# Kernel optimization log

Measured on AMD Instinct MI355X. Metric: run time of the kernel, lower is better.

Reference implementation:

```python
import jax, jax.numpy as jnp
import numpy as np

COLOR_SIZE = 4
SIZE = 64
FILTERS = 512
LENGTH = SIZE * SIZE * 3  # 12288


def setup_inputs() -> dict:
    key = jax.random.key(0)
    k1, k2, k3 = jax.random.split(key, 3)
    example = jax.random.randint(k1, (8, SIZE, SIZE, 3), 0, COLOR_SIZE, dtype=jnp.int32)
    kernel = jax.random.normal(k2, (FILTERS, LENGTH), dtype=jnp.float32)
    bias = jnp.zeros((FILTERS,), dtype=jnp.float32)
    dense_w = jax.random.normal(k3, (FILTERS, COLOR_SIZE), dtype=jnp.float32) * 0.02
    dense_b = jnp.zeros((COLOR_SIZE,), dtype=jnp.float32)
    return {"example": example, "kernel": kernel, "bias": bias,
            "dense_w": dense_w, "dense_b": dense_b}


def reference(example, kernel, bias, dense_w, dense_b):
    B = example.shape[0]
    L = kernel.shape[1]  # 12288
    # normalize int pixels to [-1, 1)
    x = example.astype(jnp.float32) / COLOR_SIZE * 2.0 - 1.0
    x = x.reshape(B, L)                                   # [B, L]
    # FFT-based long (causal full) convolution, fft_length = 2L
    Xf = jnp.fft.rfft(x, n=2 * L, axis=-1)                # [B, L+1] complex64
    Kf = jnp.fft.rfft(kernel, n=2 * L, axis=-1)           # [F, L+1]
    y = jnp.fft.irfft(Xf[:, None, :] * Kf[None, :, :], n=2 * L, axis=-1)[..., :L]  # [B, F, L]
    y = jnp.transpose(y, (0, 2, 1)) + bias                # [B, L, F]
    y = jax.nn.relu(y)
    out = y @ dense_w + dense_b                           # [B, L, color_size]
    return out.reshape(B, SIZE, SIZE, 3, COLOR_SIZE).astype(jnp.float32)
```

## Files before the change

kernel.cpp:

```cpp
#include <hip/hip_runtime.h>

#define FF 512
#define LL 12288
#define NJC 1556
#define NR 128

typedef _Float16 half8 __attribute__((ext_vector_type(8)));
typedef float    f32x4 __attribute__((ext_vector_type(4)));

__global__ __launch_bounds__(256) void build_At(const float* __restrict__ kern,
                                                _Float16* __restrict__ At) {
    int tid  = blockIdx.x * 256 + threadIdx.x;
    int lane = tid & 63;
    int rest = tid >> 6;
    int dc   = rest % 384;
    int ft   = rest / 384;
    int f    = ft * 16 + (lane & 15);
    int d0   = dc * 32 + (lane >> 4) * 8;
    const float* src = kern + (size_t)f * LL + d0;
    half8 v;
#pragma unroll
    for (int i = 0; i < 8; ++i) v[i] = (_Float16)src[i];
    ((half8*)At)[tid] = v;
}

__global__ __launch_bounds__(256) void build_XB(const int* __restrict__ ex,
                                                _Float16* __restrict__ XB) {
    int tid = blockIdx.x * 256 + threadIdx.x;
    if (tid >= NJC * NR) return;
    int r  = tid & 127;
    int jc = tid >> 7;
    int s  = r >> 3, b = r & 7;
    int j0 = jc * 8;
    half8 v;
#pragma unroll
    for (int i = 0; i < 8; ++i) {
        int idx = LL - 1 - (j0 + i) - s;
        float x = 0.f;
        if (idx >= 0) x = (float)ex[b * LL + idx] * 0.5f - 1.0f;
        v[i] = (_Float16)x;
    }
    ((half8*)XB)[tid] = v;
}

__global__ __launch_bounds__(256) void init_out(const float* __restrict__ db,
                                                float* __restrict__ out) {
    int tid = blockIdx.x * 256 + threadIdx.x;
    out[tid] = db[tid & 3];
}

__device__ __forceinline__ void gl_lds16(const half8* g, half8* l) {
    __builtin_amdgcn_global_load_lds((const __attribute__((address_space(1))) void*)g,
                                     (__attribute__((address_space(3))) void*)l, 16, 0, 0);
}

__global__ __launch_bounds__(256, 2) void conv_main(const _Float16* __restrict__ At,
                                                    const _Float16* __restrict__ XB,
                                                    const float* __restrict__ bias,
                                                    const float* __restrict__ dw,
                                                    float* __restrict__ out) {
    __shared__ half8 Abuf[2][4][8][64];

    int bx    = blockIdx.x;
    int slot  = bx & 7;
    int f_blk = slot >> 1;
    int n_blk = 383 - ((bx >> 3) * 2 + (slot & 1));
    int n0 = n_blk << 5;
    int M  = (n_blk + 4) >> 2;

    int tid  = threadIdx.x;
    int lane = tid & 63;
    int wid  = tid >> 6;
    int quad = lane >> 4;
    int bb   = lane & 7;
    int nh   = (lane >> 3) & 1;

    const half8* Ag  = (const half8*)At;
    const half8* ag0 = Ag + ((size_t)(f_blk * 8 + wid) * 384) * 64 + lane;
    const half8* ag1 = Ag + ((size_t)(f_blk * 8 + wid + 4) * 384) * 64 + lane;

    const half8* Bg = (const half8*)XB;
    int jc0 = 1534 - 4 * n_blk + quad - 2 * nh;
    const half8* pB[4];
#pragma unroll
    for (int t = 0; t < 4; ++t) {
        int tt = wid * 4 + t;
        int r  = (15 - tt) * 8 + bb;
        pB[t] = Bg + (size_t)jc0 * 128 + r;
    }

    f32x4 acc[8][4];
#pragma unroll
    for (int r8 = 0; r8 < 8; ++r8)
#pragma unroll
        for (int t = 0; t < 4; ++t) acc[r8][t] = (f32x4){0.f, 0.f, 0.f, 0.f};

#pragma unroll
    for (int sub = 0; sub < 4; ++sub) {
        gl_lds16(ag0 + (size_t)sub * 64, &Abuf[0][sub][wid][lane]);
        gl_lds16(ag1 + (size_t)sub * 64, &Abuf[0][sub][wid + 4][lane]);
    }
    half8 bcur[4], bnxt[4];
#pragma unroll
    for (int t = 0; t < 4; ++t) bcur[t] = pB[t][0];
    __syncthreads();

    for (int mc = 0; mc < M; ++mc) {
        int buf = mc & 1;
        if (mc + 1 < M) {
            size_t oa = (size_t)(mc + 1) * 256;
#pragma unroll
            for (int sub = 0; sub < 4; ++sub) {
                gl_lds16(ag0 + oa + (size_t)sub * 64, &Abuf[buf ^ 1][sub][wid][lane]);
                gl_lds16(ag1 + oa + (size_t)sub * 64, &Abuf[buf ^ 1][sub][wid + 4][lane]);
            }
        }
#pragma unroll
        for (int sub = 0; sub < 4; ++sub) {
            int dc = mc * 4 + sub;
            size_t ob = (size_t)(dc + 1) * 512;
#pragma unroll
            for (int t = 0; t < 4; ++t) bnxt[t] = pB[t][ob];
            half8 a[8];
#pragma unroll
            for (int r8 = 0; r8 < 8; ++r8) a[r8] = Abuf[buf][sub][r8][lane];
#pragma unroll
            for (int r8 = 0; r8 < 8; ++r8)
#pragma unroll
                for (int t = 0; t < 4; ++t)
                    acc[r8][t] = __builtin_amdgcn_mfma_f32_16x16x32_f16(a[r8], bcur[t], acc[r8][t], 0, 0, 0);
#pragma unroll
            for (int t = 0; t < 4; ++t) bcur[t] = bnxt[t];
        }
        __syncthreads();
    }

    float p[4][4] = {{0.f}};
#pragma unroll
    for (int r8 = 0; r8 < 8; ++r8) {
#pragma unroll
        for (int reg = 0; reg < 4; ++reg) {
            int f = f_blk * 128 + r8 * 16 + quad * 4 + reg;
            float bs = bias[f];
            float4 w = *(const float4*)(dw + (size_t)f * 4);
#pragma unroll
            for (int t = 0; t < 4; ++t) {
                float y = fmaxf(acc[r8][t][reg] + bs, 0.f);
                p[t][0] += y * w.x; p[t][1] += y * w.y;
                p[t][2] += y * w.z; p[t][3] += y * w.w;
            }
        }
    }
#pragma unroll
    for (int t = 0; t < 4; ++t)
#pragma unroll
        for (int c = 0; c < 4; ++c) {
            float v = p[t][c];
            v += __shfl_xor(v, 16, 64);
            v += __shfl_xor(v, 32, 64);
            p[t][c] = v;
        }
    if (quad == 0) {
#pragma unroll
        for (int t = 0; t < 4; ++t) {
            int n = n0 + (wid * 4 + t) + 16 * nh;
            float* o = out + ((size_t)bb * LL + n) * 4;
#pragma unroll
            for (int c = 0; c < 4; ++c) atomicAdd(o + c, p[t][c]);
        }
    }
}

extern "C" void kernel_launch(void* const* d_in, const int* in_sizes, int n_in,
                              void* d_out, int out_size, void* d_ws, size_t ws_size,
                              hipStream_t stream) {
    const int*   ex   = (const int*)d_in[0];
    const float* kern = (const float*)d_in[1];
    const float* bias = (const float*)d_in[2];
    const float* dw   = (const float*)d_in[3];
    const float* db   = (const float*)d_in[4];
    float* out = (float*)d_out;

    _Float16* At = (_Float16*)d_ws;
    _Float16* XB = (_Float16*)((char*)d_ws + (size_t)FF * LL * 2);

    hipLaunchKernelGGL(build_At, dim3(3072), dim3(256), 0, stream, kern, At);
    hipLaunchKernelGGL(build_XB, dim3(778),  dim3(256), 0, stream, ex, XB);
    hipLaunchKernelGGL(init_out, dim3(1536), dim3(256), 0, stream, db, out);
    hipLaunchKernelGGL(conv_main, dim3(1536), dim3(256), 0, stream, At, XB, bias, dw, out);
}
```

Baseline: 520.8 us.

## Switch conv GEMM to 32x32x16 MFMA tiles with 2x2 wave layout

Replaces the 16x16x32 MFMA tiling with 32x32x16 MFMA instructions. The A operand is re-laid out in the prebuilt fp16 kernel matrix and LDS, and each wave now covers 64 filters by 32 output columns instead of 128 filters by 16 columns. Each MFMA does more work per operand load, and each wave reads only two A fragments per k-step instead of eight, which lowers LDS traffic per FLOP. The cost is re-deriving the B/X pointer indexing and the epilogue filter mapping, which risks indexing errors and changes register pressure.

New measurement: 562.9 us. 8.1% more time.

```diff
diff --git a/kernel.cpp b/kernel.cpp
--- a/kernel.cpp
+++ b/kernel.cpp
@@ -6,17 +6,17 @@
 #define NR 128
 
 typedef _Float16 half8 __attribute__((ext_vector_type(8)));
-typedef float    f32x4 __attribute__((ext_vector_type(4)));
+typedef float    f32x16 __attribute__((ext_vector_type(16)));
 
 __global__ __launch_bounds__(256) void build_At(const float* __restrict__ kern,
                                                 _Float16* __restrict__ At) {
     int tid  = blockIdx.x * 256 + threadIdx.x;
     int lane = tid & 63;
     int rest = tid >> 6;
-    int dc   = rest % 384;
-    int ft   = rest / 384;
-    int f    = ft * 16 + (lane & 15);
-    int d0   = dc * 32 + (lane >> 4) * 8;
+    int kc   = rest % 768;
+    int fgt  = rest / 768;
+    int f    = fgt * 32 + (lane & 31);
+    int d0   = kc * 16 + (lane >> 5) * 8;
     const float* src = kern + (size_t)f * LL + d0;
     half8 v;
 #pragma unroll
@@ -59,7 +59,7 @@
                                                     const float* __restrict__ bias,
                                                     const float* __restrict__ dw,
                                                     float* __restrict__ out) {
-    __shared__ half8 Abuf[2][4][8][64];
+    __shared__ half8 Abuf[2][8][4][64];
 
     int bx    = blockIdx.x;
     int slot  = bx & 7;
@@ -71,102 +71,109 @@
     int tid  = threadIdx.x;
     int lane = tid & 63;
     int wid  = tid >> 6;
-    int quad = lane >> 4;
+    int wf   = wid >> 1;
+    int wc   = wid & 1;
     int bb   = lane & 7;
-    int nh   = (lane >> 3) & 1;
+    int nq   = (lane >> 3) & 3;
+    int kh   = lane >> 5;
 
-    const half8* Ag  = (const half8*)At;
-    const half8* ag0 = Ag + ((size_t)(f_blk * 8 + wid) * 384) * 64 + lane;
-    const half8* ag1 = Ag + ((size_t)(f_blk * 8 + wid + 4) * 384) * 64 + lane;
+    const half8* Ag = (const half8*)At;
+    const half8* ag[8];
+#pragma unroll
+    for (int u = 0; u < 8; ++u) {
+        int kcl = wid * 2 + (u >> 2);
+        int ft  = u & 3;
+        ag[u] = Ag + ((size_t)(f_blk * 4 + ft) * 768 + kcl) * 64 + lane;
+    }
 
     const half8* Bg = (const half8*)XB;
-    int jc0 = 1534 - 4 * n_blk + quad - 2 * nh;
     const half8* pB[4];
 #pragma unroll
-    for (int t = 0; t < 4; ++t) {
-        int tt = wid * 4 + t;
-        int r  = (15 - tt) * 8 + bb;
-        pB[t] = Bg + (size_t)jc0 * 128 + r;
+    for (int cf = 0; cf < 4; ++cf) {
+        int n  = n0 + wc * 16 + cf * 4 + nq;
+        int T  = LL - 1 - n + 8 * kh;
+        pB[cf] = Bg + (size_t)(T >> 3) * 128 + (T & 7) * 8 + bb;
     }
 
-    f32x4 acc[8][4];
+    f32x16 acc[2][4];
 #pragma unroll
-    for (int r8 = 0; r8 < 8; ++r8)
+    for (int rf = 0; rf < 2; ++rf)
 #pragma unroll
-        for (int t = 0; t < 4; ++t) acc[r8][t] = (f32x4){0.f, 0.f, 0.f, 0.f};
+        for (int cf = 0; cf < 4; ++cf)
+#pragma unroll
+            for (int i = 0; i < 16; ++i) acc[rf][cf][i] = 0.f;
 
 #pragma unroll
-    for (int sub = 0; sub < 4; ++sub) {
-        gl_lds16(ag0 + (size_t)sub * 64, &Abuf[0][sub][wid][lane]);
-        gl_lds16(ag1 + (size_t)sub * 64, &Abuf[0][sub][wid + 4][lane]);
-    }
+    for (int u = 0; u < 8; ++u)
+        gl_lds16(ag[u], &Abuf[0][wid * 2 + (u >> 2)][u & 3][lane]);
     half8 bcur[4], bnxt[4];
 #pragma unroll
-    for (int t = 0; t < 4; ++t) bcur[t] = pB[t][0];
+    for (int cf = 0; cf < 4; ++cf) bcur[cf] = pB[cf][0];
+#pragma unroll
+    for (int cf = 0; cf < 4; ++cf) pB[cf] += 256;
     __syncthreads();
 
     for (int mc = 0; mc < M; ++mc) {
         int buf = mc & 1;
         if (mc + 1 < M) {
-            size_t oa = (size_t)(mc + 1) * 256;
+            size_t oa = (size_t)(mc + 1) * 512;
 #pragma unroll
-            for (int sub = 0; sub < 4; ++sub) {
-                gl_lds16(ag0 + oa + (size_t)sub * 64, &Abuf[buf ^ 1][sub][wid][lane]);
-                gl_lds16(ag1 + oa + (size_t)sub * 64, &Abuf[buf ^ 1][sub][wid + 4][lane]);
-            }
+            for (int u = 0; u < 8; ++u)
+                gl_lds16(ag[u] + oa, &Abuf[buf ^ 1][wid * 2 + (u >> 2)][u & 3][lane]);
         }
 #pragma unroll
-        for (int sub = 0; sub < 4; ++sub) {
-            int dc = mc * 4 + sub;
-            size_t ob = (size_t)(dc + 1) * 512;
+        for (int kc = 0; kc < 8; ++kc) {
 #pragma unroll
-            for (int t = 0; t < 4; ++t) bnxt[t] = pB[t][ob];
-            half8 a[8];
+            for (int cf = 0; cf < 4; ++cf) bnxt[cf] = pB[cf][0];
 #pragma unroll
-            for (int r8 = 0; r8 < 8; ++r8) a[r8] = Abuf[buf][sub][r8][lane];
+            for (int cf = 0; cf < 4; ++cf) pB[cf] += 256;
+            half8 a0 = Abuf[buf][kc][wf * 2 + 0][lane];
+            half8 a1 = Abuf[buf][kc][wf * 2 + 1][lane];
 #pragma unroll
-            for (int r8 = 0; r8 < 8; ++r8)
+            for (int cf = 0; cf < 4; ++cf)
+                acc[0][cf] = __builtin_amdgcn_mfma_f32_32x32x16_f16(a0, bcur[cf], acc[0][cf], 0, 0, 0);
 #pragma unroll
-                for (int t = 0; t < 4; ++t)
-                    acc[r8][t] = __builtin_amdgcn_mfma_f32_16x16x32_f16(a[r8], bcur[t], acc[r8][t], 0, 0, 0);
+            for (int cf = 0; cf < 4; ++cf)
+                acc[1][cf] = __builtin_amdgcn_mfma_f32_32x32x16_f16(a1, bcur[cf], acc[1][cf], 0, 0, 0);
 #pragma unroll
-            for (int t = 0; t < 4; ++t) bcur[t] = bnxt[t];
+            for (int cf = 0; cf < 4; ++cf) bcur[cf] = bnxt[cf];
         }
         __syncthreads();
     }
 
-    float p[4][4] = {{0.f}};
+    float p[4][4];
 #pragma unroll
-    for (int r8 = 0; r8 < 8; ++r8) {
+    for (int cf = 0; cf < 4; ++cf)
 #pragma unroll
-        for (int reg = 0; reg < 4; ++reg) {
-            int f = f_blk * 128 + r8 * 16 + quad * 4 + reg;
+        for (int c = 0; c < 4; ++c) p[cf][c] = 0.f;
+
+#pragma unroll
+    for (int rf = 0; rf < 2; ++rf) {
+#pragma unroll
+        for (int reg = 0; reg < 16; ++reg) {
+            int f = f_blk * 128 + wf * 64 + rf * 32 + (reg & 3) + 8 * (reg >> 2) + 4 * kh;
             float bs = bias[f];
             float4 w = *(const float4*)(dw + (size_t)f * 4);
 #pragma unroll
-            for (int t = 0; t < 4; ++t) {
-                float y = fmaxf(acc[r8][t][reg] + bs, 0.f);
-                p[t][0] += y * w.x; p[t][1] += y * w.y;
-                p[t][2] += y * w.z; p[t][3] += y * w.w;
+            for (int cf = 0; cf < 4; ++cf) {
+                float y = fmaxf(acc[rf][cf][reg] + bs, 0.f);
+                p[cf][0] += y * w.x; p[cf][1] += y * w.y;
+                p[cf][2] += y * w.z; p[cf][3] += y * w.w;
             }
         }
     }
 #pragma unroll
-    for (int t = 0; t < 4; ++t)
+    for (int cf = 0; cf < 4; ++cf)
 #pragma unroll
-        for (int c = 0; c < 4; ++c) {
-            float v = p[t][c];
-            v += __shfl_xor(v, 16, 64);
-            v += __shfl_xor(v, 32, 64);
-            p[t][c] = v;
-        }
-    if (quad == 0) {
+        for (int c = 0; c < 4; ++c)
+            p[cf][c] += __shfl_xor(p[cf][c], 32, 64);
+    if (kh == 0) {
 #pragma unroll
-        for (int t = 0; t < 4; ++t) {
-            int n = n0 + (wid * 4 + t) + 16 * nh;
+        for (int cf = 0; cf < 4; ++cf) {
+            int n = n0 + wc * 16 + cf * 4 + nq;
             float* o = out + ((size_t)bb * LL + n) * 4;
 #pragma unroll
-            for (int c = 0; c < 4; ++c) atomicAdd(o + c, p[t][c]);
+            for (int c = 0; c < 4; ++c) atomicAdd(o + c, p[cf][c]);
         }
     }
 }
```

## Deepen A-tile LDS pipeline to four stages with partial vmcnt waits

Applied to the files above, without the earlier changes.

Restructures the main loop so each iteration processes two k-subchunks instead of four, with a 4-slot ring buffer for A tiles loaded two iterations ahead. The full __syncthreads is replaced by an s_waitcnt vmcnt(12) plus a raw barrier, so in-flight async global-to-LDS loads can stay outstanding across iterations. The aim is to hide A-load latency better. The cost is reliance on exact vmcnt counting, and it unconditionally issues loads past the useful range. It also drops the guard against prefetching beyond M, which may read past the tile or hit out-of-range memory.

Measured after the change: 523.2 us. About the same (+0.5%).

```diff
diff --git a/kernel.cpp b/kernel.cpp
--- a/kernel.cpp
+++ b/kernel.cpp
@@ -59,14 +59,14 @@
                                                     const float* __restrict__ bias,
                                                     const float* __restrict__ dw,
                                                     float* __restrict__ out) {
-    __shared__ half8 Abuf[2][4][8][64];
+    __shared__ half8 Abuf[4][2][8][64];
 
     int bx    = blockIdx.x;
     int slot  = bx & 7;
     int f_blk = slot >> 1;
     int n_blk = 383 - ((bx >> 3) * 2 + (slot & 1));
     int n0 = n_blk << 5;
-    int M  = (n_blk + 4) >> 2;
+    int U  = (n_blk + 2) >> 1;
 
     int tid  = threadIdx.x;
     int lane = tid & 63;
@@ -96,34 +96,34 @@
         for (int t = 0; t < 4; ++t) acc[r8][t] = (f32x4){0.f, 0.f, 0.f, 0.f};
 
 #pragma unroll
-    for (int sub = 0; sub < 4; ++sub) {
-        gl_lds16(ag0 + (size_t)sub * 64, &Abuf[0][sub][wid][lane]);
-        gl_lds16(ag1 + (size_t)sub * 64, &Abuf[0][sub][wid + 4][lane]);
-    }
+    for (int uu = 0; uu < 2; ++uu)
+#pragma unroll
+        for (int sub = 0; sub < 2; ++sub) {
+            gl_lds16(ag0 + (size_t)(uu * 2 + sub) * 64, &Abuf[uu][sub][wid][lane]);
+            gl_lds16(ag1 + (size_t)(uu * 2 + sub) * 64, &Abuf[uu][sub][wid + 4][lane]);
+        }
     half8 bcur[4], bnxt[4];
 #pragma unroll
-    for (int t = 0; t < 4; ++t) bcur[t] = pB[t][0];
-    __syncthreads();
+    for (int t = 0; t < 4; ++t) { bcur[t] = pB[t][0]; pB[t] += 512; }
+    asm volatile("s_waitcnt vmcnt(0)" ::: "memory");
+    __builtin_amdgcn_s_barrier();
 
-    for (int mc = 0; mc < M; ++mc) {
-        int buf = mc & 1;
-        if (mc + 1 < M) {
-            size_t oa = (size_t)(mc + 1) * 256;
+    for (int u = 0; u < U; ++u) {
+        int rs = (u + 2) & 3;
+        size_t os = (size_t)(u + 2) * 128;
+        gl_lds16(ag0 + os,      &Abuf[rs][0][wid][lane]);
+        gl_lds16(ag0 + os + 64, &Abuf[rs][1][wid][lane]);
+        gl_lds16(ag1 + os,      &Abuf[rs][0][wid + 4][lane]);
+        gl_lds16(ag1 + os + 64, &Abuf[rs][1][wid + 4][lane]);
+
+        int rc = u & 3;
 #pragma unroll
-            for (int sub = 0; sub < 4; ++sub) {
-                gl_lds16(ag0 + oa + (size_t)sub * 64, &Abuf[buf ^ 1][sub][wid][lane]);
-                gl_lds16(ag1 + oa + (size_t)sub * 64, &Abuf[buf ^ 1][sub][wid + 4][lane]);
-            }
-        }
+        for (int s = 0; s < 2; ++s) {
 #pragma unroll
-        for (int sub = 0; sub < 4; ++sub) {
-            int dc = mc * 4 + sub;
-            size_t ob = (size_t)(dc + 1) * 512;
-#pragma unroll
-            for (int t = 0; t < 4; ++t) bnxt[t] = pB[t][ob];
+            for (int t = 0; t < 4; ++t) { bnxt[t] = pB[t][0]; pB[t] += 512; }
             half8 a[8];
 #pragma unroll
-            for (int r8 = 0; r8 < 8; ++r8) a[r8] = Abuf[buf][sub][r8][lane];
+            for (int r8 = 0; r8 < 8; ++r8) a[r8] = Abuf[rc][s][r8][lane];
 #pragma unroll
             for (int r8 = 0; r8 < 8; ++r8)
 #pragma unroll
@@ -132,7 +132,9 @@
 #pragma unroll
             for (int t = 0; t < 4; ++t) bcur[t] = bnxt[t];
         }
-        __syncthreads();
+
+        asm volatile("s_waitcnt vmcnt(12)" ::: "memory");
+        __builtin_amdgcn_s_barrier();
     }
 
     float p[4][4] = {{0.f}};
```
